# Performance work log

Measured on AMD Instinct MI355X. Metric: run time of the kernel, lower is better.

## Reference

```python
import jax, jax.numpy as jnp
import numpy as np

EPS = 1e-5

def _mlp(x, W1, b1, W2, b2):
    h = jax.nn.gelu(x @ W1 + b1, approximate=False)
    return h @ W2 + b2

def _ln(x, g, b):
    m = jnp.mean(x, axis=-1, keepdims=True)
    v = jnp.mean((x - m) ** 2, axis=-1, keepdims=True)
    return (x - m) * jax.lax.rsqrt(v + EPS) * g + b

def setup_inputs() -> dict:
    key = jax.random.key(0)
    B, N, D = 4, 256, 128
    ks = jax.random.split(key, 32)
    s = 0.02
    inp = {
        "node_h": jax.random.normal(ks[0], (B, N, D), jnp.float32),
        "pair_h": jax.random.normal(ks[1], (B, N, N, D), jnp.float32),
        "node_mask": jax.random.randint(ks[2], (B, N), 0, 2, jnp.int32),
        "edge_mask": jax.random.randint(ks[3], (B, N, N), 0, 2, jnp.int32),
        # node_from_pair MLP: 3D -> 2D -> D
        "nfp_W1": jax.random.normal(ks[4], (3 * D, 2 * D), jnp.float32) * s,
        "nfp_b1": jnp.zeros((2 * D,), jnp.float32),
        "nfp_W2": jax.random.normal(ks[5], (2 * D, D), jnp.float32) * s,
        "nfp_b2": jnp.zeros((D,), jnp.float32),
        # pair_from_node MLP: 5D -> 2D -> D
        "pfn_W1": jax.random.normal(ks[6], (5 * D, 2 * D), jnp.float32) * s,
        "pfn_b1": jnp.zeros((2 * D,), jnp.float32),
        "pfn_W2": jax.random.normal(ks[7], (2 * D, D), jnp.float32) * s,
        "pfn_b2": jnp.zeros((D,), jnp.float32),
        # node_ff: D -> 4D -> D
        "nff_W1": jax.random.normal(ks[8], (D, 4 * D), jnp.float32) * s,
        "nff_b1": jnp.zeros((4 * D,), jnp.float32),
        "nff_W2": jax.random.normal(ks[9], (4 * D, D), jnp.float32) * s,
        "nff_b2": jnp.zeros((D,), jnp.float32),
        # pair_ff: D -> 4D -> D
        "pff_W1": jax.random.normal(ks[10], (D, 4 * D), jnp.float32) * s,
        "pff_b1": jnp.zeros((4 * D,), jnp.float32),
        "pff_W2": jax.random.normal(ks[11], (4 * D, D), jnp.float32) * s,
        "pff_b2": jnp.zeros((D,), jnp.float32),
        # gates: 2D -> D, sigmoid
        "og_W": jax.random.normal(ks[12], (2 * D, D), jnp.float32) * s,
        "og_b": jnp.zeros((D,), jnp.float32),
        "ig_W": jax.random.normal(ks[13], (2 * D, D), jnp.float32) * s,
        "ig_b": jnp.zeros((D,), jnp.float32),
        # LayerNorms
        "nn1_g": jnp.ones((D,), jnp.float32), "nn1_b": jnp.zeros((D,), jnp.float32),
        "nn2_g": jnp.ones((D,), jnp.float32), "nn2_b": jnp.zeros((D,), jnp.float32),
        "pn1_g": jnp.ones((D,), jnp.float32), "pn1_b": jnp.zeros((D,), jnp.float32),
        "pn2_g": jnp.ones((D,), jnp.float32), "pn2_b": jnp.zeros((D,), jnp.float32),
    }
    return inp

def reference(node_h, pair_h, node_mask, edge_mask,
              nfp_W1, nfp_b1, nfp_W2, nfp_b2,
              pfn_W1, pfn_b1, pfn_W2, pfn_b2,
              nff_W1, nff_b1, nff_W2, nff_b2,
              pff_W1, pff_b1, pff_W2, pff_b2,
              og_W, og_b, ig_W, ig_b,
              nn1_g, nn1_b, nn2_g, nn2_b,
              pn1_g, pn1_b, pn2_g, pn2_b):
    vp = edge_mask.astype(jnp.float32)                       # [B,N,N]
    pair_m = pair_h * vp[..., None]                          # masked pairs
    out_deg = jnp.clip(vp.sum(axis=2), 1.0)[..., None]       # [B,N,1]
    in_deg = jnp.clip(vp.sum(axis=1), 1.0)[..., None]        # [B,N,1]
    out_ctx_raw = pair_m.sum(axis=2) / out_deg               # [B,N,D]
    in_ctx_raw = pair_m.sum(axis=1) / in_deg                 # [B,N,D]
    out_g = jax.nn.sigmoid(jnp.concatenate([node_h, out_ctx_raw], -1) @ og_W + og_b)
    in_g = jax.nn.sigmoid(jnp.concatenate([node_h, in_ctx_raw], -1) @ ig_W + ig_b)
    node_upd = _mlp(jnp.concatenate([node_h, out_g * out_ctx_raw, in_g * in_ctx_raw], -1),
                    nfp_W1, nfp_b1, nfp_W2, nfp_b2)
    node_h = _ln(node_h + node_upd, nn1_g, nn1_b)
    node_h = _ln(node_h + _mlp(node_h, nff_W1, nff_b1, nff_W2, nff_b2), nn2_g, nn2_b)
    node_h = node_h * node_mask.astype(jnp.float32)[..., None]

    B, N, D = node_h.shape
    hi = jnp.broadcast_to(node_h[:, :, None, :], (B, N, N, D))
    hj = jnp.broadcast_to(node_h[:, None, :, :], (B, N, N, D))
    feat = jnp.concatenate([pair_h, hi, hj, hi - hj, hi * hj], -1)  # [B,N,N,5D]
    pair_upd = _mlp(feat, pfn_W1, pfn_b1, pfn_W2, pfn_b2)
    pair_h = _ln(pair_h + pair_upd, pn1_g, pn1_b)
    pair_h = _ln(pair_h + _mlp(pair_h, pff_W1, pff_b1, pff_W2, pff_b2), pn2_g, pn2_b)
    pair_h = pair_h * vp[..., None]
    return (node_h, pair_h)
```

## Files before the change

kernel.cpp:

```cpp
#include <hip/hip_runtime.h>
#include <hip/hip_bf16.h>

#define DI __device__ __forceinline__

typedef float f32x4 __attribute__((ext_vector_type(4)));
typedef float f32x2 __attribute__((ext_vector_type(2)));
typedef short s16x8 __attribute__((ext_vector_type(8)));
typedef short s16x4 __attribute__((ext_vector_type(4)));
typedef unsigned u32x2 __attribute__((ext_vector_type(2)));
typedef unsigned u32x4 __attribute__((ext_vector_type(4)));

DI short f2bf(float x) {
  union { float f; unsigned u; } v; v.f = x;
  unsigned r = v.u + 0x7fffu + ((v.u >> 16) & 1u);
  return (short)(r >> 16);
}

DI float bf2f(short x) {
  union { unsigned u; float f; } v;
  v.u = ((unsigned)(unsigned short)x) << 16;
  return v.f;
}

DI unsigned cvt_pk(float lo, float hi) {
  unsigned r;
  asm("v_cvt_pk_bf16_f32 %0, %1, %2" : "=v"(r) : "v"(lo), "v"(hi));
  return r;
}

DI s16x8 pack8(f32x4 a, f32x4 b) {
  union { u32x4 u; s16x8 s; } r;
  r.u[0] = cvt_pk(a[0], a[1]); r.u[1] = cvt_pk(a[2], a[3]);
  r.u[2] = cvt_pk(b[0], b[1]); r.u[3] = cvt_pk(b[2], b[3]);
  return r.s;
}

DI float gelu_f(float x) {
  const float e = __expf(-x * fmaf(x * x, 0.0713548162f, 1.5957691216f));
  return __fdividef(x, 1.f + e);
}

__global__ __launch_bounds__(256) void prep_ctx_kernel(
    const float* __restrict__ pair_h, const int* __restrict__ edge_mask,
    const float* __restrict__ pfnW1, const float* __restrict__ pfnW2,
    const float* __restrict__ pffW1, const float* __restrict__ pffW2,
    short* __restrict__ W1b, float* __restrict__ Wu, short* __restrict__ W2T,
    short* __restrict__ W1Tp, short* __restrict__ W2Tp,
    float* __restrict__ out_ctx, float* __restrict__ in_ctx) {
  __shared__ float sacc[2][128];
  __shared__ float sdeg[2];
  const int t = threadIdx.x;
  if (blockIdx.x >= 2048) {
    int idx = (blockIdx.x - 2048) * 256 + t;
    if (idx < 98304) {
      int n = idx / 384, k = idx % 384;
      float v;
      if (k < 128) v = pfnW1[k * 256 + n];
      else if (k < 256) v = pfnW1[(128 + k) * 256 + n] - pfnW1[(256 + k) * 256 + n];
      else v = pfnW1[(256 + k) * 256 + n];
      W1b[idx] = f2bf(v);
      return;
    }
    idx -= 98304;
    if (idx < 32768) {
      int k = idx / 256, n = idx % 256;
      Wu[idx] = pfnW1[(128 + k) * 256 + n] + pfnW1[(384 + k) * 256 + n];
      return;
    }
    idx -= 32768;
    if (idx < 32768) {
      int n = idx / 256, k = idx % 256;
      W2T[idx] = f2bf(pfnW2[k * 128 + n]);
      return;
    }
    idx -= 32768;
    if (idx < 65536) {
      int n = idx / 128, k = idx % 128;
      W1Tp[idx] = f2bf(pffW1[k * 512 + n]);
      return;
    }
    idx -= 65536;
    if (idx < 65536) {
      int n = idx / 512, k = idx % 512;
      W2Tp[idx] = f2bf(pffW2[k * 128 + n]);
    }
    return;
  }
  const int wg = blockIdx.x;
  const int half = t >> 7, d = t & 127;
  const bool outmode = wg < 1024;
  const int w2 = outmode ? wg : wg - 1024;
  const int b = w2 >> 8, x = w2 & 255;
  float acc = 0.f, deg = 0.f;
  for (int y0 = 0; y0 < 256; y0 += 2) {
    const int y = y0 + half;
    int row;
    if (outmode) row = (b * 256 + x) * 256 + y;
    else row = (b * 256 + y) * 256 + x;
    const int m = edge_mask[row];
    if (m) {
      acc += pair_h[(long)row * 128 + d];
      deg += 1.f;
    }
  }
  sacc[half][d] = acc;
  if (d == 0) sdeg[half] = deg;
  __syncthreads();
  if (t < 128) {
    float tot = sacc[0][d] + sacc[1][d];
    float dg = fmaxf(sdeg[0] + sdeg[1], 1.f);
    float* dst = outmode ? out_ctx : in_ctx;
    dst[(b * 256 + x) * 128 + d] = tot / dg;
  }
}

__global__ __launch_bounds__(256) void node_kernel(
    const float* __restrict__ node_h, const float* __restrict__ out_ctx,
    const float* __restrict__ in_ctx, const int* __restrict__ node_mask,
    const float* __restrict__ ogW, const float* __restrict__ ogb,
    const float* __restrict__ igW, const float* __restrict__ igb,
    const float* __restrict__ nW1, const float* __restrict__ nb1,
    const float* __restrict__ nW2, const float* __restrict__ nb2,
    const float* __restrict__ fW1, const float* __restrict__ fb1,
    const float* __restrict__ fW2, const float* __restrict__ fb2,
    const float* __restrict__ g1, const float* __restrict__ be1,
    const float* __restrict__ g2, const float* __restrict__ be2,
    const float* __restrict__ Wu, const float* __restrict__ ub1,
    float* __restrict__ out_node, short* __restrict__ node_bf,
    float* __restrict__ u_all) {
  __shared__ float sh[4][1792];
  __shared__ float fin[8][128];
  const int t = threadIdx.x;
  const int wv = t >> 6, lane = t & 63;
  float* const xn = sh[wv];
  float* const xo = sh[wv] + 256;
  float* const xi = sh[wv] + 512;
  float* const hh = sh[wv] + 768;
  const int row0 = blockIdx.x * 8 + wv * 2;

#pragma unroll
  for (int r = 0; r < 2; ++r) {
    const int row = row0 + r;
#pragma unroll
    for (int c = 0; c < 2; ++c) {
      const int col = lane + 64 * c;
      xn[r * 128 + col] = node_h[row * 128 + col];
      xo[r * 128 + col] = out_ctx[row * 128 + col];
      xi[r * 128 + col] = in_ctx[row * 128 + col];
    }
  }
  __syncthreads();

  {
    float ao[2][2], ai[2][2];
#pragma unroll
    for (int c = 0; c < 2; ++c) {
      const int col = lane + 64 * c;
      ao[0][c] = ao[1][c] = ogb[col];
      ai[0][c] = ai[1][c] = igb[col];
    }
    for (int k = 0; k < 256; ++k) {
      float xo0, xo1, xi0, xi1;
      if (k < 128) {
        xo0 = xi0 = xn[k];
        xo1 = xi1 = xn[128 + k];
      } else {
        xo0 = xo[k - 128]; xo1 = xo[k];
        xi0 = xi[k - 128]; xi1 = xi[k];
      }
#pragma unroll
      for (int c = 0; c < 2; ++c) {
        const int col = lane + 64 * c;
        const float wo = ogW[k * 128 + col], wi = igW[k * 128 + col];
        ao[0][c] += xo0 * wo; ao[1][c] += xo1 * wo;
        ai[0][c] += xi0 * wi; ai[1][c] += xi1 * wi;
      }
    }
#pragma unroll
    for (int c = 0; c < 2; ++c) {
      const int col = lane + 64 * c;
#pragma unroll
      for (int r = 0; r < 2; ++r) {
        const float go = 1.f / (1.f + __expf(-ao[r][c]));
        const float gi = 1.f / (1.f + __expf(-ai[r][c]));
        xo[r * 128 + col] *= go;
        xi[r * 128 + col] *= gi;
      }
    }
  }
  __syncthreads();

  {
    float a1[2][4];
#pragma unroll
    for (int c = 0; c < 4; ++c) {
      const int col = lane + 64 * c;
      a1[0][c] = a1[1][c] = nb1[col];
    }
    for (int k = 0; k < 384; ++k) {
      const float* src = (k < 128) ? xn : (k < 256) ? xo : xi;
      const int kk = k & 127;
      const float x0 = src[kk], x1 = src[128 + kk];
#pragma unroll
      for (int c = 0; c < 4; ++c) {
        const int col = lane + 64 * c;
        const float w = nW1[k * 256 + col];
        a1[0][c] += x0 * w; a1[1][c] += x1 * w;
      }
    }
#pragma unroll
    for (int c = 0; c < 4; ++c) {
      const int col = lane + 64 * c;
      hh[col] = gelu_f(a1[0][c]);
      hh[512 + col] = gelu_f(a1[1][c]);
    }
  }
  __syncthreads();
  {
    float a2[2][2];
#pragma unroll
    for (int c = 0; c < 2; ++c) {
      const int col = lane + 64 * c;
      a2[0][c] = a2[1][c] = nb2[col];
    }
    for (int k = 0; k < 256; ++k) {
      const float h0 = hh[k], h1 = hh[512 + k];
#pragma unroll
      for (int c = 0; c < 2; ++c) {
        const int col = lane + 64 * c;
        const float w = nW2[k * 128 + col];
        a2[0][c] += h0 * w; a2[1][c] += h1 * w;
      }
    }
#pragma unroll
    for (int r = 0; r < 2; ++r) {
      float v0 = xn[r * 128 + lane] + a2[r][0];
      float v1 = xn[r * 128 + lane + 64] + a2[r][1];
      float s = v0 + v1, ss = v0 * v0 + v1 * v1;
#pragma unroll
      for (int off = 1; off < 64; off <<= 1) {
        s += __shfl_xor(s, off, 64);
        ss += __shfl_xor(ss, off, 64);
      }
      const float m = s * (1.f / 128.f);
      const float var = ss * (1.f / 128.f) - m * m;
      const float rs = rsqrtf(var + 1e-5f);
      xn[r * 128 + lane] = (v0 - m) * rs * g1[lane] + be1[lane];
      xn[r * 128 + lane + 64] = (v1 - m) * rs * g1[lane + 64] + be1[lane + 64];
    }
  }
  __syncthreads();

  {
    float af[2][8];
#pragma unroll
    for (int c = 0; c < 8; ++c) {
      const int col = lane + 64 * c;
      af[0][c] = af[1][c] = fb1[col];
    }
    for (int k = 0; k < 128; ++k) {
      const float x0 = xn[k], x1 = xn[128 + k];
#pragma unroll
      for (int c = 0; c < 8; ++c) {
        const int col = lane + 64 * c;
        const float w = fW1[k * 512 + col];
        af[0][c] += x0 * w; af[1][c] += x1 * w;
      }
    }
#pragma unroll
    for (int c = 0; c < 8; ++c) {
      const int col = lane + 64 * c;
      hh[col] = gelu_f(af[0][c]);
      hh[512 + col] = gelu_f(af[1][c]);
    }
  }
  __syncthreads();
  {
    float a2[2][2];
#pragma unroll
    for (int c = 0; c < 2; ++c) {
      const int col = lane + 64 * c;
      a2[0][c] = a2[1][c] = fb2[col];
    }
    for (int k = 0; k < 512; ++k) {
      const float h0 = hh[k], h1 = hh[512 + k];
#pragma unroll
      for (int c = 0; c < 2; ++c) {
        const int col = lane + 64 * c;
        const float w = fW2[k * 128 + col];
        a2[0][c] += h0 * w; a2[1][c] += h1 * w;
      }
    }
#pragma unroll
    for (int r = 0; r < 2; ++r) {
      const int row = row0 + r;
      float v0 = xn[r * 128 + lane] + a2[r][0];
      float v1 = xn[r * 128 + lane + 64] + a2[r][1];
      float s = v0 + v1, ss = v0 * v0 + v1 * v1;
#pragma unroll
      for (int off = 1; off < 64; off <<= 1) {
        s += __shfl_xor(s, off, 64);
        ss += __shfl_xor(ss, off, 64);
      }
      const float m = s * (1.f / 128.f);
      const float var = ss * (1.f / 128.f) - m * m;
      const float rs = rsqrtf(var + 1e-5f);
      const float msk = (float)node_mask[row];
      const float o0 = ((v0 - m) * rs * g2[lane] + be2[lane]) * msk;
      const float o1 = ((v1 - m) * rs * g2[lane + 64] + be2[lane + 64]) * msk;
      out_node[row * 128 + lane] = o0;
      out_node[row * 128 + lane + 64] = o1;
      node_bf[row * 128 + lane] = f2bf(o0);
      node_bf[row * 128 + lane + 64] = f2bf(o1);
      fin[wv * 2 + r][lane] = o0;
      fin[wv * 2 + r][lane + 64] = o1;
    }
  }
  __syncthreads();
  {
    float uacc[8];
    const float bb = ub1[t];
#pragma unroll
    for (int r = 0; r < 8; ++r) uacc[r] = bb;
#pragma unroll 4
    for (int k = 0; k < 128; ++k) {
      const float w = Wu[k * 256 + t];
#pragma unroll
      for (int r = 0; r < 8; ++r) uacc[r] += fin[r][k] * w;
    }
#pragma unroll
    for (int r = 0; r < 8; ++r)
      u_all[(blockIdx.x * 8 + r) * 256 + t] = uacc[r];
  }
}

__global__ __launch_bounds__(512, 4) void pair_kernel(
    const float* __restrict__ pair_h, const short* __restrict__ node_bf,
    const int* __restrict__ edge_mask, const short* __restrict__ W1b,
    const short* __restrict__ W2T, const short* __restrict__ W1Tp,
    const short* __restrict__ W2Tp, const float* __restrict__ u_all,
    const float* __restrict__ b2, const float* __restrict__ b1p,
    const float* __restrict__ b2p, const float* __restrict__ g1,
    const float* __restrict__ be1, const float* __restrict__ g2,
    const float* __restrict__ be2, float* __restrict__ out_pair) {
  constexpr int OFF_A = 0, OFF_H1 = 0, OFF_Y = 0, OFF_H2 = 16384,
                OFF_SCR = 49152;
  __shared__ __align__(16) char smem[51200];

  const int t = threadIdx.x;
  const int wg = blockIdx.x;
  const int b = wg >> 10, rem = wg & 1023;
  const int i = rem >> 2, j0 = (rem & 3) << 6;
  const int bi = (b << 8) + i;
  const long rowbase = (long)bi * 256 + j0;

  const int lane = t & 63, wv = t >> 6;
  const int lr = lane & 15, lq = lane >> 4;
  const int swz = (lr & 7) << 4;

  {
    const int r = t >> 3, oc = t & 7, c0 = oc * 16;
    const int rsw = (r & 7) << 4;
    const float* prow = pair_h + (rowbase + r) * 128 + c0;
    const short* hjrow = node_bf + (b * 256 + j0 + r) * 128 + c0;
    const short* hirow = node_bf + (b * 256 + i) * 128 + c0;
    char* arow = smem + OFF_A + r * 768;
#pragma unroll
    for (int h = 0; h < 2; ++h) {
      f32x4 p0 = *(const f32x4*)(prow + h * 8);
      f32x4 p1 = *(const f32x4*)(prow + h * 8 + 4);
      s16x8 hj = *(const s16x8*)(hjrow + h * 8);
      s16x8 hi = *(const s16x8*)(hirow + h * 8);
      *(s16x8*)(arow + ((c0 * 2 + h * 16) ^ rsw)) = pack8(p0, p1);
      *(s16x8*)(arow + ((256 + c0 * 2 + h * 16) ^ rsw)) = hj;
      union { u32x4 u; s16x8 s; } pd;
#pragma unroll
      for (int e = 0; e < 4; ++e)
        pd.u[e] = cvt_pk(bf2f(hi[2 * e]) * bf2f(hj[2 * e]),
                         bf2f(hi[2 * e + 1]) * bf2f(hj[2 * e + 1]));
      *(s16x8*)(arow + ((512 + c0 * 2 + h * 16) ^ rsw)) = pd.s;
    }
  }
  __syncthreads();

  f32x4 acc1[4][2];
#pragma unroll
  for (int jt = 0; jt < 4; ++jt)
#pragma unroll
    for (int nt = 0; nt < 2; ++nt) acc1[jt][nt] = {0.f, 0.f, 0.f, 0.f};
  {
    const int nb = wv * 32;
    const short* wp0 = W1b + (nb + lr) * 384 + lq * 8;
    const short* wp1 = W1b + (nb + 16 + lr) * 384 + lq * 8;
    s16x8 w0 = *(const s16x8*)wp0;
    s16x8 w1 = *(const s16x8*)wp1;
#pragma unroll
    for (int ks = 0; ks < 12; ++ks) {
      s16x8 nw0 = w0, nw1 = w1;
      if (ks < 11) {
        nw0 = *(const s16x8*)(wp0 + (ks + 1) * 32);
        nw1 = *(const s16x8*)(wp1 + (ks + 1) * 32);
      }
      s16x8 d[4];
#pragma unroll
      for (int jt = 0; jt < 4; ++jt)
        d[jt] = *(const s16x8*)(smem + OFF_A +
                                (((jt * 16 + lr) * 768 + ks * 64 + lq * 16) ^ swz));
#pragma unroll
      for (int jt = 0; jt < 4; ++jt) {
        acc1[jt][0] = __builtin_amdgcn_mfma_f32_16x16x32_bf16(w0, d[jt], acc1[jt][0], 0, 0, 0);
        acc1[jt][1] = __builtin_amdgcn_mfma_f32_16x16x32_bf16(w1, d[jt], acc1[jt][1], 0, 0, 0);
      }
      w0 = nw0; w1 = nw1;
    }
  }
  __syncthreads();
  {
    const int nb = wv * 32;
#pragma unroll
    for (int nt = 0; nt < 2; ++nt) {
      const int n0 = nb + nt * 16 + lq * 4;
      f32x4 bu = *(const f32x4*)(u_all + bi * 256 + n0);
#pragma unroll
      for (int jt = 0; jt < 4; ++jt) {
        const int j = jt * 16 + lr;
        u32x2 pk = {cvt_pk(gelu_f(acc1[jt][nt][0] + bu[0]),
                           gelu_f(acc1[jt][nt][1] + bu[1])),
                    cvt_pk(gelu_f(acc1[jt][nt][2] + bu[2]),
                           gelu_f(acc1[jt][nt][3] + bu[3]))};
        *(u32x2*)(smem + OFF_H1 + ((j * 512 + n0 * 2) ^ swz)) = pk;
      }
    }
  }
  __syncthreads();

  const int jb = (wv >> 2) * 32, nb2 = (wv & 3) * 32;
  f32x4 x1v[2][2];
  {
    f32x4 acc2[2][2];
#pragma unroll
    for (int jt = 0; jt < 2; ++jt)
#pragma unroll
      for (int nt = 0; nt < 2; ++nt) acc2[jt][nt] = {0.f, 0.f, 0.f, 0.f};
    const short* wp0 = W2T + (nb2 + lr) * 256 + lq * 8;
    const short* wp1 = W2T + (nb2 + 16 + lr) * 256 + lq * 8;
    s16x8 w0 = *(const s16x8*)wp0;
    s16x8 w1 = *(const s16x8*)wp1;
#pragma unroll
    for (int ks = 0; ks < 8; ++ks) {
      s16x8 nw0 = w0, nw1 = w1;
      if (ks < 7) {
        nw0 = *(const s16x8*)(wp0 + (ks + 1) * 32);
        nw1 = *(const s16x8*)(wp1 + (ks + 1) * 32);
      }
      s16x8 d[2];
#pragma unroll
      for (int jt = 0; jt < 2; ++jt)
        d[jt] = *(const s16x8*)(smem + OFF_H1 +
                                (((jb + jt * 16 + lr) * 512 + ks * 64 + lq * 16) ^ swz));
#pragma unroll
      for (int jt = 0; jt < 2; ++jt) {
        acc2[jt][0] = __builtin_amdgcn_mfma_f32_16x16x32_bf16(w0, d[jt], acc2[jt][0], 0, 0, 0);
        acc2[jt][1] = __builtin_amdgcn_mfma_f32_16x16x32_bf16(w1, d[jt], acc2[jt][1], 0, 0, 0);
      }
      w0 = nw0; w1 = nw1;
    }
#pragma unroll
    for (int nt = 0; nt < 2; ++nt) {
      const int n0 = nb2 + nt * 16 + lq * 4;
      f32x4 bv = *(const f32x4*)(b2 + n0);
#pragma unroll
      for (int jt = 0; jt < 2; ++jt) {
        const int j = jb + jt * 16 + lr;
        f32x4 pr = *(const f32x4*)(pair_h + (rowbase + j) * 128 + n0);
        x1v[jt][nt] = acc2[jt][nt] + bv + pr;
      }
    }
  }
  {
    float s[2], ss[2];
#pragma unroll
    for (int jt = 0; jt < 2; ++jt) {
      s[jt] = 0.f; ss[jt] = 0.f;
#pragma unroll
      for (int nt = 0; nt < 2; ++nt)
#pragma unroll
        for (int v = 0; v < 4; ++v) {
          const float x = x1v[jt][nt][v];
          s[jt] += x; ss[jt] += x * x;
        }
      s[jt] += __shfl_xor(s[jt], 16, 64);
      ss[jt] += __shfl_xor(ss[jt], 16, 64);
      s[jt] += __shfl_xor(s[jt], 32, 64);
      ss[jt] += __shfl_xor(ss[jt], 32, 64);
    }
    if (lq == 0) {
#pragma unroll
      for (int jt = 0; jt < 2; ++jt) {
        const int j = jb + jt * 16 + lr;
        f32x2 p = {s[jt], ss[jt]};
        *(f32x2*)(smem + OFF_SCR + j * 32 + (wv & 3) * 8) = p;
      }
    }
    __syncthreads();
    float lnm[2], lnr[2];
#pragma unroll
    for (int jt = 0; jt < 2; ++jt) {
      const int j = jb + jt * 16 + lr;
      f32x4 pA = *(const f32x4*)(smem + OFF_SCR + j * 32);
      f32x4 pB = *(const f32x4*)(smem + OFF_SCR + j * 32 + 16);
      const float S = pA[0] + pA[2] + pB[0] + pB[2];
      const float SS = pA[1] + pA[3] + pB[1] + pB[3];
      const float m = S * (1.f / 128.f);
      const float var = SS * (1.f / 128.f) - m * m;
      lnm[jt] = m;
      lnr[jt] = rsqrtf(var + 1e-5f);
    }
#pragma unroll
    for (int nt = 0; nt < 2; ++nt) {
      const int n0 = nb2 + nt * 16 + lq * 4;
      f32x4 gv = *(const f32x4*)(g1 + n0);
      f32x4 bv = *(const f32x4*)(be1 + n0);
#pragma unroll
      for (int jt = 0; jt < 2; ++jt) {
        const int j = jb + jt * 16 + lr;
        float y[4];
#pragma unroll
        for (int v = 0; v < 4; ++v)
          y[v] = (x1v[jt][nt][v] - lnm[jt]) * lnr[jt] * gv[v] + bv[v];
        u32x2 pk = {cvt_pk(y[0], y[1]), cvt_pk(y[2], y[3])};
        *(u32x2*)(smem + OFF_Y + ((j * 256 + n0 * 2) ^ swz)) = pk;
      }
    }
  }
  __syncthreads();

  f32x4 acc4[2][2];
#pragma unroll
  for (int jt = 0; jt < 2; ++jt)
#pragma unroll
    for (int nt = 0; nt < 2; ++nt) acc4[jt][nt] = {0.f, 0.f, 0.f, 0.f};

#pragma unroll
  for (int p = 0; p < 2; ++p) {
    f32x4 acc3[4][2];
#pragma unroll
    for (int jt = 0; jt < 4; ++jt)
#pragma unroll
      for (int nt = 0; nt < 2; ++nt) acc3[jt][nt] = {0.f, 0.f, 0.f, 0.f};
    {
      const int nb3 = p * 256 + wv * 32;
      const short* wp0 = W1Tp + (nb3 + lr) * 128 + lq * 8;
      const short* wp1 = W1Tp + (nb3 + 16 + lr) * 128 + lq * 8;
#pragma unroll
      for (int ks = 0; ks < 4; ++ks) {
        s16x8 w0 = *(const s16x8*)(wp0 + ks * 32);
        s16x8 w1 = *(const s16x8*)(wp1 + ks * 32);
        s16x8 d[4];
#pragma unroll
        for (int jt = 0; jt < 4; ++jt)
          d[jt] = *(const s16x8*)(smem + OFF_Y +
                                  (((jt * 16 + lr) * 256 + ks * 64 + lq * 16) ^ swz));
#pragma unroll
        for (int jt = 0; jt < 4; ++jt) {
          acc3[jt][0] = __builtin_amdgcn_mfma_f32_16x16x32_bf16(w0, d[jt], acc3[jt][0], 0, 0, 0);
          acc3[jt][1] = __builtin_amdgcn_mfma_f32_16x16x32_bf16(w1, d[jt], acc3[jt][1], 0, 0, 0);
        }
      }
    }
    if (p == 1) __syncthreads();
    {
#pragma unroll
      for (int nt = 0; nt < 2; ++nt) {
        const int n0l = wv * 32 + nt * 16 + lq * 4;
        f32x4 bv = *(const f32x4*)(b1p + p * 256 + n0l);
#pragma unroll
        for (int jt = 0; jt < 4; ++jt) {
          const int j = jt * 16 + lr;
          u32x2 pk = {cvt_pk(gelu_f(acc3[jt][nt][0] + bv[0]),
                             gelu_f(acc3[jt][nt][1] + bv[1])),
                      cvt_pk(gelu_f(acc3[jt][nt][2] + bv[2]),
                             gelu_f(acc3[jt][nt][3] + bv[3]))};
          *(u32x2*)(smem + OFF_H2 + ((j * 512 + n0l * 2) ^ swz)) = pk;
        }
      }
    }
    __syncthreads();
    {
      const short* qp0 = W2Tp + (nb2 + lr) * 512 + p * 256 + lq * 8;
      const short* qp1 = W2Tp + (nb2 + 16 + lr) * 512 + p * 256 + lq * 8;
#pragma unroll
      for (int ks = 0; ks < 8; ++ks) {
        s16x8 w0 = *(const s16x8*)(qp0 + ks * 32);
        s16x8 w1 = *(const s16x8*)(qp1 + ks * 32);
        s16x8 d[2];
#pragma unroll
        for (int jt = 0; jt < 2; ++jt)
          d[jt] = *(const s16x8*)(smem + OFF_H2 +
                                  (((jb + jt * 16 + lr) * 512 + ks * 64 + lq * 16) ^ swz));
#pragma unroll
        for (int jt = 0; jt < 2; ++jt) {
          acc4[jt][0] = __builtin_amdgcn_mfma_f32_16x16x32_bf16(w0, d[jt], acc4[jt][0], 0, 0, 0);
          acc4[jt][1] = __builtin_amdgcn_mfma_f32_16x16x32_bf16(w1, d[jt], acc4[jt][1], 0, 0, 0);
        }
      }
    }
  }

  f32x4 x2v[2][2];
#pragma unroll
  for (int nt = 0; nt < 2; ++nt) {
    const int n0 = nb2 + nt * 16 + lq * 4;
    f32x4 bv = *(const f32x4*)(b2p + n0);
#pragma unroll
    for (int jt = 0; jt < 2; ++jt) {
      const int j = jb + jt * 16 + lr;
      s16x4 yv = *(const s16x4*)(smem + OFF_Y + ((j * 256 + n0 * 2) ^ swz));
      f32x4 yr;
#pragma unroll
      for (int v = 0; v < 4; ++v) yr[v] = bf2f(yv[v]);
      x2v[jt][nt] = acc4[jt][nt] + bv + yr;
    }
  }
  {
    float s[2], ss[2];
#pragma unroll
    for (int jt = 0; jt < 2; ++jt) {
      s[jt] = 0.f; ss[jt] = 0.f;
#pragma unroll
      for (int nt = 0; nt < 2; ++nt)
#pragma unroll
        for (int v = 0; v < 4; ++v) {
          const float x = x2v[jt][nt][v];
          s[jt] += x; ss[jt] += x * x;
        }
      s[jt] += __shfl_xor(s[jt], 16, 64);
      ss[jt] += __shfl_xor(ss[jt], 16, 64);
      s[jt] += __shfl_xor(s[jt], 32, 64);
      ss[jt] += __shfl_xor(ss[jt], 32, 64);
    }
    __syncthreads();
    if (lq == 0) {
#pragma unroll
      for (int jt = 0; jt < 2; ++jt) {
        const int j = jb + jt * 16 + lr;
        f32x2 p = {s[jt], ss[jt]};
        *(f32x2*)(smem + OFF_SCR + j * 32 + (wv & 3) * 8) = p;
      }
    }
    __syncthreads();
    float lnm[2], lnr[2], vp[2];
#pragma unroll
    for (int jt = 0; jt < 2; ++jt) {
      const int j = jb + jt * 16 + lr;
      f32x4 pA = *(const f32x4*)(smem + OFF_SCR + j * 32);
      f32x4 pB = *(const f32x4*)(smem + OFF_SCR + j * 32 + 16);
      const float S = pA[0] + pA[2] + pB[0] + pB[2];
      const float SS = pA[1] + pA[3] + pB[1] + pB[3];
      const float m = S * (1.f / 128.f);
      const float var = SS * (1.f / 128.f) - m * m;
      lnm[jt] = m;
      lnr[jt] = rsqrtf(var + 1e-5f);
      vp[jt] = (float)edge_mask[(long)bi * 256 + j0 + j];
    }
#pragma unroll
    for (int nt = 0; nt < 2; ++nt) {
      const int n0 = nb2 + nt * 16 + lq * 4;
      f32x4 gv = *(const f32x4*)(g2 + n0);
      f32x4 bv = *(const f32x4*)(be2 + n0);
#pragma unroll
      for (int jt = 0; jt < 2; ++jt) {
        const int j = jb + jt * 16 + lr;
        f32x4 o;
#pragma unroll
        for (int v = 0; v < 4; ++v)
          o[v] = ((x2v[jt][nt][v] - lnm[jt]) * lnr[jt] * gv[v] + bv[v]) * vp[jt];
        *(f32x4*)(out_pair + (rowbase + j) * 128 + n0) = o;
      }
    }
  }
}

extern "C" void kernel_launch(void* const* d_in, const int* in_sizes, int n_in,
                              void* d_out, int out_size, void* d_ws,
                              size_t ws_size, hipStream_t stream) {
  const float* node_h = (const float*)d_in[0];
  const float* pair_h = (const float*)d_in[1];
  const int* node_mask = (const int*)d_in[2];
  const int* edge_mask = (const int*)d_in[3];
  const float* nfp_W1 = (const float*)d_in[4];
  const float* nfp_b1 = (const float*)d_in[5];
  const float* nfp_W2 = (const float*)d_in[6];
  const float* nfp_b2 = (const float*)d_in[7];
  const float* pfn_W1 = (const float*)d_in[8];
  const float* pfn_b1 = (const float*)d_in[9];
  const float* pfn_W2 = (const float*)d_in[10];
  const float* pfn_b2 = (const float*)d_in[11];
  const float* nff_W1 = (const float*)d_in[12];
  const float* nff_b1 = (const float*)d_in[13];
  const float* nff_W2 = (const float*)d_in[14];
  const float* nff_b2 = (const float*)d_in[15];
  const float* pff_W1 = (const float*)d_in[16];
  const float* pff_b1 = (const float*)d_in[17];
  const float* pff_W2 = (const float*)d_in[18];
  const float* pff_b2 = (const float*)d_in[19];
  const float* og_W = (const float*)d_in[20];
  const float* og_b = (const float*)d_in[21];
  const float* ig_W = (const float*)d_in[22];
  const float* ig_b = (const float*)d_in[23];
  const float* nn1_g = (const float*)d_in[24];
  const float* nn1_b = (const float*)d_in[25];
  const float* nn2_g = (const float*)d_in[26];
  const float* nn2_b = (const float*)d_in[27];
  const float* pn1_g = (const float*)d_in[28];
  const float* pn1_b = (const float*)d_in[29];
  const float* pn2_g = (const float*)d_in[30];
  const float* pn2_b = (const float*)d_in[31];

  char* ws = (char*)d_ws;
  short* W1b = (short*)(ws);
  short* W2T = (short*)(ws + 196608);
  short* W1Tp = (short*)(ws + 262144);
  short* W2Tp = (short*)(ws + 393216);
  float* Wu = (float*)(ws + 524288);
  float* out_ctx = (float*)(ws + 655360);
  float* in_ctx = (float*)(ws + 1179648);
  short* node_bf = (short*)(ws + 1703936);
  float* u_all = (float*)(ws + 1966080);

  float* out_node = (float*)d_out;
  float* out_pair = (float*)d_out + 131072;

  prep_ctx_kernel<<<3200, 256, 0, stream>>>(
      pair_h, edge_mask, pfn_W1, pfn_W2, pff_W1, pff_W2, W1b, Wu, W2T, W1Tp,
      W2Tp, out_ctx, in_ctx);
  node_kernel<<<128, 256, 0, stream>>>(
      node_h, out_ctx, in_ctx, node_mask, og_W, og_b, ig_W, ig_b, nfp_W1,
      nfp_b1, nfp_W2, nfp_b2, nff_W1, nff_b1, nff_W2, nff_b2, nn1_g, nn1_b,
      nn2_g, nn2_b, Wu, pfn_b1, out_node, node_bf, u_all);
  pair_kernel<<<4096, 512, 0, stream>>>(
      pair_h, node_bf, edge_mask, W1b, W2T, W1Tp, W2Tp, u_all, pfn_b2, pff_b1,
      pff_b2, pn1_g, pn1_b, pn2_g, pn2_b, out_pair);
}
```

Baseline: 631.2 us.

## Halve pair_kernel tile to 32 rows with 256-thread blocks for higher occupancy

The pair kernel now processes 32 j-rows per block with 4 waves instead of 64 rows with 8 waves. Blocks are twice as many and LDS use is halved. Each wave loops over two 128-column halves of the hidden dimension, and weight loads in the pair-FF matmuls are now software prefetched. One barrier is moved or dropped to allow more resident blocks per CU. The cost is that each weight fragment is reused across fewer rows, so weight traffic per output row doubles.

```diff
diff --git a/kernel.cpp b/kernel.cpp
--- a/kernel.cpp
+++ b/kernel.cpp
@@ -334,7 +334,7 @@
   }
 }
 
-__global__ __launch_bounds__(512, 4) void pair_kernel(
+__global__ __launch_bounds__(256, 6) void pair_kernel(
     const float* __restrict__ pair_h, const short* __restrict__ node_bf,
     const int* __restrict__ edge_mask, const short* __restrict__ W1b,
     const short* __restrict__ W2T, const short* __restrict__ W1Tp,
@@ -343,14 +343,14 @@
     const float* __restrict__ b2p, const float* __restrict__ g1,
     const float* __restrict__ be1, const float* __restrict__ g2,
     const float* __restrict__ be2, float* __restrict__ out_pair) {
-  constexpr int OFF_A = 0, OFF_H1 = 0, OFF_Y = 0, OFF_H2 = 16384,
-                OFF_SCR = 49152;
-  __shared__ __align__(16) char smem[51200];
+  constexpr int OFF_A = 0, OFF_H1 = 0, OFF_Y = 0, OFF_H2 = 8192,
+                OFF_SCR = 24576;
+  __shared__ __align__(16) char smem[25600];
 
   const int t = threadIdx.x;
   const int wg = blockIdx.x;
-  const int b = wg >> 10, rem = wg & 1023;
-  const int i = rem >> 2, j0 = (rem & 3) << 6;
+  const int b = wg >> 11, rem = wg & 2047;
+  const int i = rem >> 3, j0 = (rem & 7) << 5;
   const int bi = (b << 8) + i;
   const long rowbase = (long)bi * 256 + j0;
 
@@ -383,13 +383,16 @@
   }
   __syncthreads();
 
-  f32x4 acc1[4][2];
-#pragma unroll
-  for (int jt = 0; jt < 4; ++jt)
-#pragma unroll
-    for (int nt = 0; nt < 2; ++nt) acc1[jt][nt] = {0.f, 0.f, 0.f, 0.f};
-  {
-    const int nb = wv * 32;
+  f32x4 acc1[2][2][2];
+#pragma unroll
+  for (int q = 0; q < 2; ++q)
+#pragma unroll
+    for (int jt = 0; jt < 2; ++jt)
+#pragma unroll
+      for (int nt = 0; nt < 2; ++nt) acc1[q][jt][nt] = {0.f, 0.f, 0.f, 0.f};
+#pragma unroll
+  for (int q = 0; q < 2; ++q) {
+    const int nb = q * 128 + wv * 32;
     const short* wp0 = W1b + (nb + lr) * 384 + lq * 8;
     const short* wp1 = W1b + (nb + 16 + lr) * 384 + lq * 8;
     s16x8 w0 = *(const s16x8*)wp0;
@@ -401,40 +404,41 @@
         nw0 = *(const s16x8*)(wp0 + (ks + 1) * 32);
         nw1 = *(const s16x8*)(wp1 + (ks + 1) * 32);
       }
-      s16x8 d[4];
-#pragma unroll
-      for (int jt = 0; jt < 4; ++jt)
+      s16x8 d[2];
+#pragma unroll
+      for (int jt = 0; jt < 2; ++jt)
         d[jt] = *(const s16x8*)(smem + OFF_A +
                                 (((jt * 16 + lr) * 768 + ks * 64 + lq * 16) ^ swz));
 #pragma unroll
-      for (int jt = 0; jt < 4; ++jt) {
-        acc1[jt][0] = __builtin_amdgcn_mfma_f32_16x16x32_bf16(w0, d[jt], acc1[jt][0], 0, 0, 0);
-        acc1[jt][1] = __builtin_amdgcn_mfma_f32_16x16x32_bf16(w1, d[jt], acc1[jt][1], 0, 0, 0);
+      for (int jt = 0; jt < 2; ++jt) {
+        acc1[q][jt][0] = __builtin_amdgcn_mfma_f32_16x16x32_bf16(w0, d[jt], acc1[q][jt][0], 0, 0, 0);
+        acc1[q][jt][1] = __builtin_amdgcn_mfma_f32_16x16x32_bf16(w1, d[jt], acc1[q][jt][1], 0, 0, 0);
       }
       w0 = nw0; w1 = nw1;
     }
   }
   __syncthreads();
   {
-    const int nb = wv * 32;
-#pragma unroll
-    for (int nt = 0; nt < 2; ++nt) {
-      const int n0 = nb + nt * 16 + lq * 4;
-      f32x4 bu = *(const f32x4*)(u_all + bi * 256 + n0);
-#pragma unroll
-      for (int jt = 0; jt < 4; ++jt) {
-        const int j = jt * 16 + lr;
-        u32x2 pk = {cvt_pk(gelu_f(acc1[jt][nt][0] + bu[0]),
-                           gelu_f(acc1[jt][nt][1] + bu[1])),
-                    cvt_pk(gelu_f(acc1[jt][nt][2] + bu[2]),
-                           gelu_f(acc1[jt][nt][3] + bu[3]))};
-        *(u32x2*)(smem + OFF_H1 + ((j * 512 + n0 * 2) ^ swz)) = pk;
-      }
-    }
-  }
-  __syncthreads();
-
-  const int jb = (wv >> 2) * 32, nb2 = (wv & 3) * 32;
+#pragma unroll
+    for (int q = 0; q < 2; ++q)
+#pragma unroll
+      for (int nt = 0; nt < 2; ++nt) {
+        const int n0 = q * 128 + wv * 32 + nt * 16 + lq * 4;
+        f32x4 bu = *(const f32x4*)(u_all + bi * 256 + n0);
+#pragma unroll
+        for (int jt = 0; jt < 2; ++jt) {
+          const int j = jt * 16 + lr;
+          u32x2 pk = {cvt_pk(gelu_f(acc1[q][jt][nt][0] + bu[0]),
+                             gelu_f(acc1[q][jt][nt][1] + bu[1])),
+                      cvt_pk(gelu_f(acc1[q][jt][nt][2] + bu[2]),
+                             gelu_f(acc1[q][jt][nt][3] + bu[3]))};
+          *(u32x2*)(smem + OFF_H1 + ((j * 512 + n0 * 2) ^ swz)) = pk;
+        }
+      }
+  }
+  __syncthreads();
+
+  const int nb2 = wv * 32;
   f32x4 x1v[2][2];
   {
     f32x4 acc2[2][2];
@@ -457,7 +461,7 @@
 #pragma unroll
       for (int jt = 0; jt < 2; ++jt)
         d[jt] = *(const s16x8*)(smem + OFF_H1 +
-                                (((jb + jt * 16 + lr) * 512 + ks * 64 + lq * 16) ^ swz));
+                                (((jt * 16 + lr) * 512 + ks * 64 + lq * 16) ^ swz));
 #pragma unroll
       for (int jt = 0; jt < 2; ++jt) {
         acc2[jt][0] = __builtin_amdgcn_mfma_f32_16x16x32_bf16(w0, d[jt], acc2[jt][0], 0, 0, 0);
@@ -471,7 +475,7 @@
       f32x4 bv = *(const f32x4*)(b2 + n0);
 #pragma unroll
       for (int jt = 0; jt < 2; ++jt) {
-        const int j = jb + jt * 16 + lr;
+        const int j = jt * 16 + lr;
         f32x4 pr = *(const f32x4*)(pair_h + (rowbase + j) * 128 + n0);
         x1v[jt][nt] = acc2[jt][nt] + bv + pr;
       }
@@ -497,16 +501,16 @@
     if (lq == 0) {
 #pragma unroll
       for (int jt = 0; jt < 2; ++jt) {
-        const int j = jb + jt * 16 + lr;
+        const int j = jt * 16 + lr;
         f32x2 p = {s[jt], ss[jt]};
-        *(f32x2*)(smem + OFF_SCR + j * 32 + (wv & 3) * 8) = p;
+        *(f32x2*)(smem + OFF_SCR + j * 32 + wv * 8) = p;
       }
     }
     __syncthreads();
     float lnm[2], lnr[2];
 #pragma unroll
     for (int jt = 0; jt < 2; ++jt) {
-      const int j = jb + jt * 16 + lr;
+      const int j = jt * 16 + lr;
       f32x4 pA = *(const f32x4*)(smem + OFF_SCR + j * 32);
       f32x4 pB = *(const f32x4*)(smem + OFF_SCR + j * 32 + 16);
       const float S = pA[0] + pA[2] + pB[0] + pB[2];
@@ -523,7 +527,7 @@
       f32x4 bv = *(const f32x4*)(be1 + n0);
 #pragma unroll
       for (int jt = 0; jt < 2; ++jt) {
-        const int j = jb + jt * 16 + lr;
+        const int j = jt * 16 + lr;
         float y[4];
 #pragma unroll
         for (int v = 0; v < 4; ++v)
@@ -543,39 +547,44 @@
 
 #pragma unroll
   for (int p = 0; p < 2; ++p) {
-    f32x4 acc3[4][2];
-#pragma unroll
-    for (int jt = 0; jt < 4; ++jt)
-#pragma unroll
-      for (int nt = 0; nt < 2; ++nt) acc3[jt][nt] = {0.f, 0.f, 0.f, 0.f};
-    {
-      const int nb3 = p * 256 + wv * 32;
+#pragma unroll
+    for (int qq = 0; qq < 2; ++qq) {
+      f32x4 acc3[2][2];
+#pragma unroll
+      for (int jt = 0; jt < 2; ++jt)
+#pragma unroll
+        for (int nt = 0; nt < 2; ++nt) acc3[jt][nt] = {0.f, 0.f, 0.f, 0.f};
+      const int nb3 = p * 256 + qq * 128 + wv * 32;
       const short* wp0 = W1Tp + (nb3 + lr) * 128 + lq * 8;
       const short* wp1 = W1Tp + (nb3 + 16 + lr) * 128 + lq * 8;
+      s16x8 w0 = *(const s16x8*)wp0;
+      s16x8 w1 = *(const s16x8*)wp1;
 #pragma unroll
       for (int ks = 0; ks < 4; ++ks) {
-        s16x8 w0 = *(const s16x8*)(wp0 + ks * 32);
-        s16x8 w1 = *(const s16x8*)(wp1 + ks * 32);
-        s16x8 d[4];
-#pragma unroll
-        for (int jt = 0; jt < 4; ++jt)
+        s16x8 nw0 = w0, nw1 = w1;
+        if (ks < 3) {
+          nw0 = *(const s16x8*)(wp0 + (ks + 1) * 32);
+          nw1 = *(const s16x8*)(wp1 + (ks + 1) * 32);
+        }
+        s16x8 d[2];
+#pragma unroll
+        for (int jt = 0; jt < 2; ++jt)
           d[jt] = *(const s16x8*)(smem + OFF_Y +
                                   (((jt * 16 + lr) * 256 + ks * 64 + lq * 16) ^ swz));
 #pragma unroll
-        for (int jt = 0; jt < 4; ++jt) {
+        for (int jt = 0; jt < 2; ++jt) {
           acc3[jt][0] = __builtin_amdgcn_mfma_f32_16x16x32_bf16(w0, d[jt], acc3[jt][0], 0, 0, 0);
           acc3[jt][1] = __builtin_amdgcn_mfma_f32_16x16x32_bf16(w1, d[jt], acc3[jt][1], 0, 0, 0);
         }
-      }
-    }
-    if (p == 1) __syncthreads();
-    {
+        w0 = nw0; w1 = nw1;
+      }
+      const int nbl = qq * 128 + wv * 32;
 #pragma unroll
       for (int nt = 0; nt < 2; ++nt) {
-        const int n0l = wv * 32 + nt * 16 + lq * 4;
+        const int n0l = nbl + nt * 16 + lq * 4;
         f32x4 bv = *(const f32x4*)(b1p + p * 256 + n0l);
 #pragma unroll
-        for (int jt = 0; jt < 4; ++jt) {
+        for (int jt = 0; jt < 2; ++jt) {
           const int j = jt * 16 + lr;
           u32x2 pk = {cvt_pk(gelu_f(acc3[jt][nt][0] + bv[0]),
                              gelu_f(acc3[jt][nt][1] + bv[1])),
@@ -589,22 +598,29 @@
     {
       const short* qp0 = W2Tp + (nb2 + lr) * 512 + p * 256 + lq * 8;
       const short* qp1 = W2Tp + (nb2 + 16 + lr) * 512 + p * 256 + lq * 8;
+      s16x8 w0 = *(const s16x8*)qp0;
+      s16x8 w1 = *(const s16x8*)qp1;
 #pragma unroll
       for (int ks = 0; ks < 8; ++ks) {
-        s16x8 w0 = *(const s16x8*)(qp0 + ks * 32);
-        s16x8 w1 = *(const s16x8*)(qp1 + ks * 32);
+        s16x8 nw0 = w0, nw1 = w1;
+        if (ks < 7) {
+          nw0 = *(const s16x8*)(qp0 + (ks + 1) * 32);
+          nw1 = *(const s16x8*)(qp1 + (ks + 1) * 32);
+        }
         s16x8 d[2];
 #pragma unroll
         for (int jt = 0; jt < 2; ++jt)
           d[jt] = *(const s16x8*)(smem + OFF_H2 +
-                                  (((jb + jt * 16 + lr) * 512 + ks * 64 + lq * 16) ^ swz));
+                                  (((jt * 16 + lr) * 512 + ks * 64 + lq * 16) ^ swz));
 #pragma unroll
         for (int jt = 0; jt < 2; ++jt) {
           acc4[jt][0] = __builtin_amdgcn_mfma_f32_16x16x32_bf16(w0, d[jt], acc4[jt][0], 0, 0, 0);
           acc4[jt][1] = __builtin_amdgcn_mfma_f32_16x16x32_bf16(w1, d[jt], acc4[jt][1], 0, 0, 0);
         }
-      }
-    }
+        w0 = nw0; w1 = nw1;
+      }
+    }
+    if (p == 0) __syncthreads();
   }
 
   f32x4 x2v[2][2];
@@ -614,7 +630,7 @@
     f32x4 bv = *(const f32x4*)(b2p + n0);
 #pragma unroll
     for (int jt = 0; jt < 2; ++jt) {
-      const int j = jb + jt * 16 + lr;
+      const int j = jt * 16 + lr;
       s16x4 yv = *(const s16x4*)(smem + OFF_Y + ((j * 256 + n0 * 2) ^ swz));
       f32x4 yr;
 #pragma unroll
@@ -639,20 +655,19 @@
       s[jt] += __shfl_xor(s[jt], 32, 64);
       ss[jt] += __shfl_xor(ss[jt], 32, 64);
     }
-    __syncthreads();
     if (lq == 0) {
 #pragma unroll
       for (int jt = 0; jt < 2; ++jt) {
-        const int j = jb + jt * 16 + lr;
+        const int j = jt * 16 + lr;
         f32x2 p = {s[jt], ss[jt]};
-        *(f32x2*)(smem + OFF_SCR + j * 32 + (wv & 3) * 8) = p;
+        *(f32x2*)(smem + OFF_SCR + j * 32 + wv * 8) = p;
       }
     }
     __syncthreads();
     float lnm[2], lnr[2], vp[2];
 #pragma unroll
     for (int jt = 0; jt < 2; ++jt) {
-      const int j = jb + jt * 16 + lr;
+      const int j = jt * 16 + lr;
       f32x4 pA = *(const f32x4*)(smem + OFF_SCR + j * 32);
       f32x4 pB = *(const f32x4*)(smem + OFF_SCR + j * 32 + 16);
       const float S = pA[0] + pA[2] + pB[0] + pB[2];
@@ -670,7 +685,7 @@
       f32x4 bv = *(const f32x4*)(be2 + n0);
 #pragma unroll
       for (int jt = 0; jt < 2; ++jt) {
-        const int j = jb + jt * 16 + lr;
+        const int j = jt * 16 + lr;
         f32x4 o;
 #pragma unroll
         for (int v = 0; v < 4; ++v)
@@ -738,7 +753,7 @@
       node_h, out_ctx, in_ctx, node_mask, og_W, og_b, ig_W, ig_b, nfp_W1,
       nfp_b1, nfp_W2, nfp_b2, nff_W1, nff_b1, nff_W2, nff_b2, nn1_g, nn1_b,
       nn2_g, nn2_b, Wu, pfn_b1, out_node, node_bf, u_all);
-  pair_kernel<<<4096, 512, 0, stream>>>(
+  pair_kernel<<<8192, 256, 0, stream>>>(
       pair_h, node_bf, edge_mask, W1b, W2T, W1Tp, W2Tp, u_all, pfn_b2, pff_b1,
       pff_b2, pn1_g, pn1_b, pn2_g, pn2_b, out_pair);
 }
```

Result: slower. 821.0 us (+30.1%).

## Deepen weight prefetch and double-buffer LDS fragments across pair-MLP GEMM stages

Applied to the files above, without the earlier changes.

Weight fragments for all four GEMM stages are now prefetched four k-steps ahead in register ring buffers, with the first loads issued before the preceding barrier. LDS operand fragments are double-buffered so the next k-step's reads overlap the current MFMAs. Residual pair_h, bias and edge_mask loads are hoisted earlier, and one redundant barrier before the final LayerNorm reduction is removed. The aim is to hide global and LDS latency behind matrix work, at the cost of higher VGPR pressure that may reduce occupancy or cause spills.

```diff
diff --git a/kernel.cpp b/kernel.cpp
--- a/kernel.cpp
+++ b/kernel.cpp
@@ -357,6 +357,7 @@
   const int lane = t & 63, wv = t >> 6;
   const int lr = lane & 15, lq = lane >> 4;
   const int swz = (lr & 7) << 4;
+  const int jb = (wv >> 2) * 32, nb2 = (wv & 3) * 32;
 
   {
     const int r = t >> 3, oc = t & 7, c0 = oc * 16;
@@ -392,35 +393,56 @@
     const int nb = wv * 32;
     const short* wp0 = W1b + (nb + lr) * 384 + lq * 8;
     const short* wp1 = W1b + (nb + 16 + lr) * 384 + lq * 8;
-    s16x8 w0 = *(const s16x8*)wp0;
-    s16x8 w1 = *(const s16x8*)wp1;
+    s16x8 w0p[4], w1p[4];
+#pragma unroll
+    for (int pf = 0; pf < 4; ++pf) {
+      w0p[pf] = *(const s16x8*)(wp0 + pf * 32);
+      w1p[pf] = *(const s16x8*)(wp1 + pf * 32);
+    }
+    s16x8 dc[4];
+#pragma unroll
+    for (int jt = 0; jt < 4; ++jt)
+      dc[jt] = *(const s16x8*)(smem + OFF_A +
+                               (((jt * 16 + lr) * 768 + lq * 16) ^ swz));
 #pragma unroll
     for (int ks = 0; ks < 12; ++ks) {
-      s16x8 nw0 = w0, nw1 = w1;
+      s16x8 w0 = w0p[ks & 3], w1 = w1p[ks & 3];
+      if (ks < 8) {
+        w0p[ks & 3] = *(const s16x8*)(wp0 + (ks + 4) * 32);
+        w1p[ks & 3] = *(const s16x8*)(wp1 + (ks + 4) * 32);
+      }
+      s16x8 d[4];
+#pragma unroll
+      for (int jt = 0; jt < 4; ++jt) d[jt] = dc[jt];
       if (ks < 11) {
-        nw0 = *(const s16x8*)(wp0 + (ks + 1) * 32);
-        nw1 = *(const s16x8*)(wp1 + (ks + 1) * 32);
-      }
-      s16x8 d[4];
-#pragma unroll
-      for (int jt = 0; jt < 4; ++jt)
-        d[jt] = *(const s16x8*)(smem + OFF_A +
-                                (((jt * 16 + lr) * 768 + ks * 64 + lq * 16) ^ swz));
+#pragma unroll
+        for (int jt = 0; jt < 4; ++jt)
+          dc[jt] = *(const s16x8*)(smem + OFF_A +
+                                   (((jt * 16 + lr) * 768 + (ks + 1) * 64 + lq * 16) ^ swz));
+      }
 #pragma unroll
       for (int jt = 0; jt < 4; ++jt) {
         acc1[jt][0] = __builtin_amdgcn_mfma_f32_16x16x32_bf16(w0, d[jt], acc1[jt][0], 0, 0, 0);
         acc1[jt][1] = __builtin_amdgcn_mfma_f32_16x16x32_bf16(w1, d[jt], acc1[jt][1], 0, 0, 0);
       }
-      w0 = nw0; w1 = nw1;
-    }
-  }
+    }
+  }
+  f32x4 bu0 = *(const f32x4*)(u_all + bi * 256 + wv * 32 + lq * 4);
+  f32x4 bu1 = *(const f32x4*)(u_all + bi * 256 + wv * 32 + 16 + lq * 4);
+  const short* q2p0 = W2T + (nb2 + lr) * 256 + lq * 8;
+  const short* q2p1 = W2T + (nb2 + 16 + lr) * 256 + lq * 8;
+  s16x8 q2w0[4], q2w1[4];
+  q2w0[0] = *(const s16x8*)q2p0;
+  q2w1[0] = *(const s16x8*)q2p1;
+  q2w0[1] = *(const s16x8*)(q2p0 + 32);
+  q2w1[1] = *(const s16x8*)(q2p1 + 32);
   __syncthreads();
   {
     const int nb = wv * 32;
 #pragma unroll
     for (int nt = 0; nt < 2; ++nt) {
       const int n0 = nb + nt * 16 + lq * 4;
-      f32x4 bu = *(const f32x4*)(u_all + bi * 256 + n0);
+      const f32x4 bu = nt ? bu1 : bu0;
 #pragma unroll
       for (int jt = 0; jt < 4; ++jt) {
         const int j = jt * 16 + lr;
@@ -434,47 +456,58 @@
   }
   __syncthreads();
 
-  const int jb = (wv >> 2) * 32, nb2 = (wv & 3) * 32;
   f32x4 x1v[2][2];
   {
+    q2w0[2] = *(const s16x8*)(q2p0 + 64);
+    q2w1[2] = *(const s16x8*)(q2p1 + 64);
+    q2w0[3] = *(const s16x8*)(q2p0 + 96);
+    q2w1[3] = *(const s16x8*)(q2p1 + 96);
+    f32x4 pr[2][2];
+#pragma unroll
+    for (int nt = 0; nt < 2; ++nt)
+#pragma unroll
+      for (int jt = 0; jt < 2; ++jt)
+        pr[jt][nt] = *(const f32x4*)(pair_h + (rowbase + jb + jt * 16 + lr) * 128 +
+                                     nb2 + nt * 16 + lq * 4);
+    s16x8 dc[2];
+#pragma unroll
+    for (int jt = 0; jt < 2; ++jt)
+      dc[jt] = *(const s16x8*)(smem + OFF_H1 +
+                               (((jb + jt * 16 + lr) * 512 + lq * 16) ^ swz));
     f32x4 acc2[2][2];
 #pragma unroll
     for (int jt = 0; jt < 2; ++jt)
 #pragma unroll
       for (int nt = 0; nt < 2; ++nt) acc2[jt][nt] = {0.f, 0.f, 0.f, 0.f};
-    const short* wp0 = W2T + (nb2 + lr) * 256 + lq * 8;
-    const short* wp1 = W2T + (nb2 + 16 + lr) * 256 + lq * 8;
-    s16x8 w0 = *(const s16x8*)wp0;
-    s16x8 w1 = *(const s16x8*)wp1;
 #pragma unroll
     for (int ks = 0; ks < 8; ++ks) {
-      s16x8 nw0 = w0, nw1 = w1;
+      s16x8 w0 = q2w0[ks & 3], w1 = q2w1[ks & 3];
+      if (ks < 4) {
+        q2w0[ks & 3] = *(const s16x8*)(q2p0 + (ks + 4) * 32);
+        q2w1[ks & 3] = *(const s16x8*)(q2p1 + (ks + 4) * 32);
+      }
+      s16x8 d[2];
+#pragma unroll
+      for (int jt = 0; jt < 2; ++jt) d[jt] = dc[jt];
       if (ks < 7) {
-        nw0 = *(const s16x8*)(wp0 + (ks + 1) * 32);
-        nw1 = *(const s16x8*)(wp1 + (ks + 1) * 32);
-      }
-      s16x8 d[2];
-#pragma unroll
-      for (int jt = 0; jt < 2; ++jt)
-        d[jt] = *(const s16x8*)(smem + OFF_H1 +
-                                (((jb + jt * 16 + lr) * 512 + ks * 64 + lq * 16) ^ swz));
+#pragma unroll
+        for (int jt = 0; jt < 2; ++jt)
+          dc[jt] = *(const s16x8*)(smem + OFF_H1 +
+                                   (((jb + jt * 16 + lr) * 512 + (ks + 1) * 64 + lq * 16) ^ swz));
+      }
 #pragma unroll
       for (int jt = 0; jt < 2; ++jt) {
         acc2[jt][0] = __builtin_amdgcn_mfma_f32_16x16x32_bf16(w0, d[jt], acc2[jt][0], 0, 0, 0);
         acc2[jt][1] = __builtin_amdgcn_mfma_f32_16x16x32_bf16(w1, d[jt], acc2[jt][1], 0, 0, 0);
       }
-      w0 = nw0; w1 = nw1;
     }
 #pragma unroll
     for (int nt = 0; nt < 2; ++nt) {
       const int n0 = nb2 + nt * 16 + lq * 4;
       f32x4 bv = *(const f32x4*)(b2 + n0);
 #pragma unroll
-      for (int jt = 0; jt < 2; ++jt) {
-        const int j = jb + jt * 16 + lr;
-        f32x4 pr = *(const f32x4*)(pair_h + (rowbase + j) * 128 + n0);
-        x1v[jt][nt] = acc2[jt][nt] + bv + pr;
-      }
+      for (int jt = 0; jt < 2; ++jt)
+        x1v[jt][nt] = acc2[jt][nt] + bv + pr[jt][nt];
     }
   }
   {
@@ -533,6 +566,15 @@
       }
     }
   }
+  const short* g3p0a = W1Tp + (wv * 32 + lr) * 128 + lq * 8;
+  const short* g3p1a = W1Tp + (wv * 32 + 16 + lr) * 128 + lq * 8;
+  s16x8 g3w0[4], g3w1[4];
+  g3w0[0] = *(const s16x8*)g3p0a;
+  g3w1[0] = *(const s16x8*)g3p1a;
+  g3w0[1] = *(const s16x8*)(g3p0a + 32);
+  g3w1[1] = *(const s16x8*)(g3p1a + 32);
+  const int em0 = edge_mask[rowbase + jb + lr];
+  const int em1 = edge_mask[rowbase + jb + 16 + lr];
   __syncthreads();
 
   f32x4 acc4[2][2];
@@ -552,10 +594,20 @@
       const int nb3 = p * 256 + wv * 32;
       const short* wp0 = W1Tp + (nb3 + lr) * 128 + lq * 8;
       const short* wp1 = W1Tp + (nb3 + 16 + lr) * 128 + lq * 8;
+      if (p == 0) {
+        g3w0[2] = *(const s16x8*)(wp0 + 64);
+        g3w1[2] = *(const s16x8*)(wp1 + 64);
+        g3w0[3] = *(const s16x8*)(wp0 + 96);
+        g3w1[3] = *(const s16x8*)(wp1 + 96);
+      } else {
+#pragma unroll
+        for (int pf = 0; pf < 4; ++pf) {
+          g3w0[pf] = *(const s16x8*)(wp0 + pf * 32);
+          g3w1[pf] = *(const s16x8*)(wp1 + pf * 32);
+        }
+      }
 #pragma unroll
       for (int ks = 0; ks < 4; ++ks) {
-        s16x8 w0 = *(const s16x8*)(wp0 + ks * 32);
-        s16x8 w1 = *(const s16x8*)(wp1 + ks * 32);
         s16x8 d[4];
 #pragma unroll
         for (int jt = 0; jt < 4; ++jt)
@@ -563,11 +615,18 @@
                                   (((jt * 16 + lr) * 256 + ks * 64 + lq * 16) ^ swz));
 #pragma unroll
         for (int jt = 0; jt < 4; ++jt) {
-          acc3[jt][0] = __builtin_amdgcn_mfma_f32_16x16x32_bf16(w0, d[jt], acc3[jt][0], 0, 0, 0);
-          acc3[jt][1] = __builtin_amdgcn_mfma_f32_16x16x32_bf16(w1, d[jt], acc3[jt][1], 0, 0, 0);
+          acc3[jt][0] = __builtin_amdgcn_mfma_f32_16x16x32_bf16(g3w0[ks], d[jt], acc3[jt][0], 0, 0, 0);
+          acc3[jt][1] = __builtin_amdgcn_mfma_f32_16x16x32_bf16(g3w1[ks], d[jt], acc3[jt][1], 0, 0, 0);
         }
       }
     }
+    const short* qp0 = W2Tp + (nb2 + lr) * 512 + p * 256 + lq * 8;
+    const short* qp1 = W2Tp + (nb2 + 16 + lr) * 512 + p * 256 + lq * 8;
+    s16x8 q4w0[4], q4w1[4];
+    q4w0[0] = *(const s16x8*)qp0;
+    q4w1[0] = *(const s16x8*)qp1;
+    q4w0[1] = *(const s16x8*)(qp0 + 32);
+    q4w1[1] = *(const s16x8*)(qp1 + 32);
     if (p == 1) __syncthreads();
     {
 #pragma unroll
@@ -587,17 +646,31 @@
     }
     __syncthreads();
     {
-      const short* qp0 = W2Tp + (nb2 + lr) * 512 + p * 256 + lq * 8;
-      const short* qp1 = W2Tp + (nb2 + 16 + lr) * 512 + p * 256 + lq * 8;
+      q4w0[2] = *(const s16x8*)(qp0 + 64);
+      q4w1[2] = *(const s16x8*)(qp1 + 64);
+      q4w0[3] = *(const s16x8*)(qp0 + 96);
+      q4w1[3] = *(const s16x8*)(qp1 + 96);
+      s16x8 dc[2];
+#pragma unroll
+      for (int jt = 0; jt < 2; ++jt)
+        dc[jt] = *(const s16x8*)(smem + OFF_H2 +
+                                 (((jb + jt * 16 + lr) * 512 + lq * 16) ^ swz));
 #pragma unroll
       for (int ks = 0; ks < 8; ++ks) {
-        s16x8 w0 = *(const s16x8*)(qp0 + ks * 32);
-        s16x8 w1 = *(const s16x8*)(qp1 + ks * 32);
+        s16x8 w0 = q4w0[ks & 3], w1 = q4w1[ks & 3];
+        if (ks < 4) {
+          q4w0[ks & 3] = *(const s16x8*)(qp0 + (ks + 4) * 32);
+          q4w1[ks & 3] = *(const s16x8*)(qp1 + (ks + 4) * 32);
+        }
         s16x8 d[2];
 #pragma unroll
-        for (int jt = 0; jt < 2; ++jt)
-          d[jt] = *(const s16x8*)(smem + OFF_H2 +
-                                  (((jb + jt * 16 + lr) * 512 + ks * 64 + lq * 16) ^ swz));
+        for (int jt = 0; jt < 2; ++jt) d[jt] = dc[jt];
+        if (ks < 7) {
+#pragma unroll
+          for (int jt = 0; jt < 2; ++jt)
+            dc[jt] = *(const s16x8*)(smem + OFF_H2 +
+                                     (((jb + jt * 16 + lr) * 512 + (ks + 1) * 64 + lq * 16) ^ swz));
+        }
 #pragma unroll
         for (int jt = 0; jt < 2; ++jt) {
           acc4[jt][0] = __builtin_amdgcn_mfma_f32_16x16x32_bf16(w0, d[jt], acc4[jt][0], 0, 0, 0);
@@ -639,7 +712,6 @@
       s[jt] += __shfl_xor(s[jt], 32, 64);
       ss[jt] += __shfl_xor(ss[jt], 32, 64);
     }
-    __syncthreads();
     if (lq == 0) {
 #pragma unroll
       for (int jt = 0; jt < 2; ++jt) {
@@ -661,7 +733,7 @@
       const float var = SS * (1.f / 128.f) - m * m;
       lnm[jt] = m;
       lnr[jt] = rsqrtf(var + 1e-5f);
-      vp[jt] = (float)edge_mask[(long)bi * 256 + j0 + j];
+      vp[jt] = (float)(jt ? em1 : em0);
     }
 #pragma unroll
     for (int nt = 0; nt < 2; ++nt) {
```

Measured after the change: 597.8 us. 5.3% less time.
